# Kernel optimization log

Measured on AMD Instinct MI355X. Metric: run time of the kernel, lower is better.

## Reference

```python
import jax, jax.numpy as jnp
import numpy as np

B, NV, NE = 32, 8192, 65536
SUBSTEPS = 8
DT = 0.01
K_SPRING = 1.0e4   # spring stiffness
CG_ITERS = 20      # fixed CG iterations for the implicit solve
EPS = 1e-12


def setup_inputs() -> dict:
    key = jax.random.key(0)
    k0, k1, k2, k3, k4, k5 = jax.random.split(key, 6)
    # small actuation signals per spring (rest-length modulation)
    input_action = jax.random.normal(k0, (B, NE), dtype=jnp.float32) * 0.05
    # random spring graph with guaranteed i != j
    edge_i = jax.random.randint(k1, (NE,), 0, NV, dtype=jnp.int32)
    off = jax.random.randint(k2, (NE,), 1, NV, dtype=jnp.int32)
    edge_j = ((edge_i + off) % NV).astype(jnp.int32)
    pos0 = jax.random.normal(k3, (B, NV, 3), dtype=jnp.float32) * 0.5
    vel0 = jnp.zeros((B, NV, 3), dtype=jnp.float32)
    # rest lengths near the initial configuration so the system starts close to equilibrium
    d0 = pos0[0, edge_i] - pos0[0, edge_j]
    rest_len = jnp.linalg.norm(d0, axis=-1) + 1e-2
    mass = jax.random.uniform(k4, (NV,), dtype=jnp.float32) + 0.5
    return {"input_action": input_action, "pos0": pos0, "vel0": vel0,
            "rest_len": rest_len, "mass": mass,
            "edge_i": edge_i, "edge_j": edge_j}


def _bdot(a, b):
    # per-batch inner product, keepdims for broadcasting: [B,1,1]
    return jnp.sum(a * b, axis=(1, 2), keepdims=True)


def _spring_force(pos, rest_eff, ei, ej):
    # pos: [B,NV,3], rest_eff: [B,NE]
    d = pos[:, ei] - pos[:, ej]                       # [B,NE,3]
    l = jnp.linalg.norm(d, axis=-1, keepdims=True)    # [B,NE,1]
    dirn = d / jnp.maximum(l, 1e-6)
    fe = -K_SPRING * (l - rest_eff[..., None]) * dirn # [B,NE,3]
    f = jnp.zeros_like(pos).at[:, ei].add(fe).at[:, ej].add(-fe)
    return f


def _matvec(x, mass, ei, ej):
    # A x = M x + dt^2 * k * L x  (graph Laplacian Hessian approximation)
    d = x[:, ei] - x[:, ej]
    Lx = jnp.zeros_like(x).at[:, ei].add(d).at[:, ej].add(-d)
    return mass[None, :, None] * x + (DT * DT * K_SPRING) * Lx


def _cg_solve(b, mass, ei, ej):
    x = jnp.zeros_like(b)
    r = b
    p = r
    rs = _bdot(r, r)

    def body(carry, _):
        x, r, p, rs = carry
        Ap = _matvec(p, mass, ei, ej)
        alpha = rs / (_bdot(p, Ap) + EPS)
        x = x + alpha * p
        r = r - alpha * Ap
        rs_new = _bdot(r, r)
        p = r + (rs_new / (rs + EPS)) * p
        return (x, r, p, rs_new), None

    (x, _, _, _), _ = jax.lax.scan(body, (x, r, p, rs), None, length=CG_ITERS)
    return x


def reference(input_action, pos0, vel0, rest_len, mass, edge_i, edge_j):
    gravity = jnp.array([0.0, -9.8, 0.0], dtype=pos0.dtype)
    rest_eff = rest_len[None, :] * (1.0 + input_action)  # actuated rest lengths [B,NE]
    m3 = mass[None, :, None]

    def step(carry, _):
        pos, vel = carry
        f = _spring_force(pos, rest_eff, edge_i, edge_j) + m3 * gravity
        b = m3 * vel + DT * f                  # implicit Euler RHS
        v_new = _cg_solve(b, mass, edge_i, edge_j)
        pos_new = pos + DT * v_new
        return (pos_new, v_new), pos_new

    _, traj = jax.lax.scan(step, (pos0, vel0), None, length=SUBSTEPS)
    # traj: [SUBSTEPS, B, NV, 3] -> [B, SUBSTEPS, NV, 3]
    return jnp.transpose(traj, (1, 0, 2, 3))
```

## Files before the change

kernel.cpp:

```cpp
#include <hip/hip_runtime.h>
#include <hip/hip_cooperative_groups.h>
#include <math.h>

namespace cg = cooperative_groups;

#define NVERT 8192
#define NEDGE 65536
#define NSUB 8
#define NCG 20
#define GRID 256
#define BLOCK 1024
#define DT 0.01f
#define KS 10000.0f
#define NGRP 16
#define GSIZE 16

struct Params {
  const float* action;
  const float* pos0;
  const float* vel0;
  const float* rest_len;
  const float* mass;
  const int* edge_i;
  const int* edge_j;
  float* out;
  float4* pos;
  float4* Q0;
  float4* Q1;
  float* rest_eff;
  int* adj_off;
  int* adjE_off;
  int* row_ptr;
  int* cursor;
  double* Pd;
  double* Gd;
  unsigned* bar;
};

union U64F4 { unsigned long long u[2]; float4 f; };
union U64D  { unsigned long long u;    double d; };

__device__ __forceinline__ float4 ld_dev(const float4* p) {
  U64F4 r;
  r.u[0] = __hip_atomic_load((const unsigned long long*)p,     __ATOMIC_RELAXED, __HIP_MEMORY_SCOPE_AGENT);
  r.u[1] = __hip_atomic_load((const unsigned long long*)p + 1, __ATOMIC_RELAXED, __HIP_MEMORY_SCOPE_AGENT);
  return r.f;
}
__device__ __forceinline__ void st_dev(float4* p, float4 v) {
  U64F4 r; r.f = v;
  __hip_atomic_store((unsigned long long*)p,     r.u[0], __ATOMIC_RELAXED, __HIP_MEMORY_SCOPE_AGENT);
  __hip_atomic_store((unsigned long long*)p + 1, r.u[1], __ATOMIC_RELAXED, __HIP_MEMORY_SCOPE_AGENT);
}
__device__ __forceinline__ double lddbl_dev(const double* p) {
  U64D r;
  r.u = __hip_atomic_load((const unsigned long long*)p, __ATOMIC_RELAXED, __HIP_MEMORY_SCOPE_AGENT);
  return r.d;
}
__device__ __forceinline__ void stdbl_dev(double* p, double v) {
  U64D r; r.d = v;
  __hip_atomic_store((unsigned long long*)p, r.u, __ATOMIC_RELAXED, __HIP_MEMORY_SCOPE_AGENT);
}

__device__ __forceinline__ float4 f4(float3 a) { return make_float4(a.x, a.y, a.z, 0.f); }

__device__ __forceinline__ void fast_bar(unsigned* bar, unsigned ep) {
  __syncthreads();
  if (threadIdx.x == 0) {
    const unsigned g = blockIdx.x >> 4;
    const unsigned old = __hip_atomic_fetch_add(bar + g * 32, 1u,
                          __ATOMIC_RELAXED, __HIP_MEMORY_SCOPE_AGENT);
    if (old == GSIZE * ep - 1) {
      const unsigned old2 = __hip_atomic_fetch_add(bar + NGRP * 32, 1u,
                             __ATOMIC_RELAXED, __HIP_MEMORY_SCOPE_AGENT);
      if (old2 == NGRP * ep - 1) {
#pragma unroll
        for (int i = 0; i < NGRP; ++i)
          __hip_atomic_store(bar + (NGRP + 1 + i) * 32, ep,
                             __ATOMIC_RELAXED, __HIP_MEMORY_SCOPE_AGENT);
      }
    }
    while (__hip_atomic_load(bar + (NGRP + 1 + (blockIdx.x >> 4)) * 32,
                             __ATOMIC_RELAXED, __HIP_MEMORY_SCOPE_AGENT) < ep)
      __builtin_amdgcn_s_sleep(1);
  }
  __syncthreads();
}

__device__ __forceinline__ void fast_bar_red(unsigned* bar, unsigned ep,
                                             const double* Pd, double* Gd, int par,
                                             int* lflag) {
  __syncthreads();
  const unsigned g = blockIdx.x >> 4;
  if (threadIdx.x == 0) {
    const unsigned old = __hip_atomic_fetch_add(bar + g * 32, 1u,
                          __ATOMIC_RELAXED, __HIP_MEMORY_SCOPE_AGENT);
    *lflag = (old == GSIZE * ep - 1);
  }
  __syncthreads();
  if (*lflag) {
    if (threadIdx.x < 96) {
      const double* base = Pd + (size_t)par * 256 * 96 + (size_t)(g * GSIZE) * 96
                           + threadIdx.x;
      double s = 0.0;
#pragma unroll
      for (int j = 0; j < GSIZE; ++j) s += lddbl_dev(base + j * 96);
      stdbl_dev(&Gd[(size_t)par * NGRP * 96 + g * 96 + threadIdx.x], s);
    }
    __syncthreads();
    if (threadIdx.x == 0) {
      const unsigned old2 = __hip_atomic_fetch_add(bar + NGRP * 32, 1u,
                             __ATOMIC_RELAXED, __HIP_MEMORY_SCOPE_AGENT);
      if (old2 == NGRP * ep - 1) {
#pragma unroll
        for (int i = 0; i < NGRP; ++i)
          __hip_atomic_store(bar + (NGRP + 1 + i) * 32, ep,
                             __ATOMIC_RELAXED, __HIP_MEMORY_SCOPE_AGENT);
      }
    }
  }
  if (threadIdx.x == 0) {
    while (__hip_atomic_load(bar + (NGRP + 1 + g) * 32,
                             __ATOMIC_RELAXED, __HIP_MEMORY_SCOPE_AGENT) < ep)
      __builtin_amdgcn_s_sleep(1);
  }
  __syncthreads();
}

__device__ __forceinline__ void publish_store(double* Pd, int par, double d0, double d1,
                                              double d2, double* lds) {
  d0 += __shfl_down(d0, 32);
  d1 += __shfl_down(d1, 32);
  d2 += __shfl_down(d2, 32);
  const int lane = threadIdx.x & 63, w = threadIdx.x >> 6;
  if (lane < 32) {
    lds[w * 96 + lane] = d0;
    lds[w * 96 + 32 + lane] = d1;
    lds[w * 96 + 64 + lane] = d2;
  }
  __syncthreads();
  if (threadIdx.x < 96) {
    double s = 0.0;
#pragma unroll
    for (int ww = 0; ww < BLOCK / 64; ++ww) s += lds[ww * 96 + threadIdx.x];
    stdbl_dev(&Pd[(size_t)par * 256 * 96 + (size_t)blockIdx.x * 96 + threadIdx.x], s);
  }
}

__device__ __forceinline__ void reduce_small(const double* Gd, int par,
                                             double* lds_part, double* lds_acc) {
  const int tid = threadIdx.x;
  if (tid < NGRP * 96)
    lds_part[tid] = lddbl_dev(Gd + (size_t)par * NGRP * 96 + tid);
  __syncthreads();
  if (tid < 96) {
    double s = 0.0;
#pragma unroll
    for (int g = 0; g < NGRP; ++g) s += lds_part[g * 96 + tid];
    lds_acc[tid] = s;
  }
  __syncthreads();
}

__global__ void __launch_bounds__(BLOCK) mass_spring_kernel(Params P) {
  cg::grid_group grid = cg::this_grid();
  __shared__ double lds_red[(BLOCK / 64) * 96];
  __shared__ double lds_part[NGRP * 96];
  __shared__ double lds_acc[96];
  __shared__ int lds_scan[BLOCK];
  __shared__ int lds_flag;

  const int tid = threadIdx.x;
  const int gtid = blockIdx.x * BLOCK + tid;
  const int b = tid & 31;
  const int v = gtid >> 5;
  const int vb = v * 32 + b;
  const int b16 = b * 16, b4 = b * 4;
  unsigned ep = 0;

  for (int i = gtid; i < NEDGE * 32; i += GRID * BLOCK) {
    const int e = i >> 5, bb = i & 31;
    P.rest_eff[e * 32 + bb] = P.rest_len[e] * (1.0f + P.action[bb * NEDGE + e]);
  }
  float3 pv, vv;
  pv.x = P.pos0[(b * NVERT + v) * 3 + 0];
  pv.y = P.pos0[(b * NVERT + v) * 3 + 1];
  pv.z = P.pos0[(b * NVERT + v) * 3 + 2];
  vv.x = P.vel0[(b * NVERT + v) * 3 + 0];
  vv.y = P.vel0[(b * NVERT + v) * 3 + 1];
  vv.z = P.vel0[(b * NVERT + v) * 3 + 2];
  st_dev(&P.pos[vb], f4(pv));
  if (gtid < NVERT) P.cursor[gtid] = 0;
  if (gtid < (2 * NGRP + 1) * 32) P.bar[gtid] = 0u;
  grid.sync();

  if (gtid < NEDGE) {
    atomicAdd(&P.cursor[P.edge_i[gtid]], 1);
    atomicAdd(&P.cursor[P.edge_j[gtid]], 1);
  }
  grid.sync();

  if (blockIdx.x == 0) {
    const int base = tid * (NVERT / BLOCK);
    int loc[NVERT / BLOCK];
    int sum = 0;
#pragma unroll
    for (int i = 0; i < NVERT / BLOCK; ++i) { loc[i] = P.cursor[base + i]; sum += loc[i]; }
    lds_scan[tid] = sum;
    __syncthreads();
    for (int off = 1; off < BLOCK; off <<= 1) {
      int t = 0;
      if (tid >= off) t = lds_scan[tid - off];
      __syncthreads();
      if (tid >= off) lds_scan[tid] += t;
      __syncthreads();
    }
    int run = lds_scan[tid] - sum;
#pragma unroll
    for (int i = 0; i < NVERT / BLOCK; ++i) {
      P.row_ptr[base + i] = run;
      P.cursor[base + i] = run;
      run += loc[i];
    }
    if (tid == BLOCK - 1) P.row_ptr[NVERT] = run;
  }
  grid.sync();

  if (gtid < NEDGE) {
    const int ei = P.edge_i[gtid], ej = P.edge_j[gtid];
    const int ai = atomicAdd(&P.cursor[ei], 1);
    P.adj_off[ai] = ej * 512; P.adjE_off[ai] = gtid * 128;
    const int aj = atomicAdd(&P.cursor[ej], 1);
    P.adj_off[aj] = ei * 512; P.adjE_off[aj] = gtid * 128;
  }
  grid.sync();

  const float m_v = P.mass[v];
  const int rbeg = P.row_ptr[v], rend = P.row_ptr[v + 1];
  const float degf = (float)(rend - rbeg);

  float4* qRd = P.Q0;
  float4* qWr = P.Q1;
  int pub = 0;

  for (int s = 0; s < NSUB; ++s) {
    float fx = 0.f, fy = 0.f, fz = 0.f;
    for (int a = rbeg; a < rend; ++a) {
      const int off = P.adj_off[a];
      const float4 pu = ld_dev((const float4*)((const char*)P.pos + off + b16));
      const float re = *(const float*)((const char*)P.rest_eff + P.adjE_off[a] + b4);
      const float dx = pv.x - pu.x, dy = pv.y - pu.y, dz = pv.z - pu.z;
      const float l = sqrtf(dx * dx + dy * dy + dz * dz);
      const float coef = -KS * (l - re) / fmaxf(l, 1e-6f);
      fx += coef * dx; fy += coef * dy; fz += coef * dz;
    }
    float3 rv;
    rv.x = m_v * vv.x + DT * fx;
    rv.y = m_v * vv.y + DT * (fy - 9.8f * m_v);
    rv.z = m_v * vv.z + DT * fz;
    st_dev(&qRd[vb], f4(rv));
    float3 xacc = make_float3(0.f, 0.f, 0.f);
    float3 pc = rv;
    float3 ap;
    float3 Sr, Sp;
    fast_bar(P.bar, ++ep);

    for (int k = 0; k < NCG; ++k) {
      if (k == 0) {
        float sx = 0.f, sy = 0.f, sz = 0.f;
#pragma unroll 4
        for (int a = rbeg; a < rend; ++a) {
          const float4 qu = ld_dev((const float4*)((const char*)qRd + P.adj_off[a] + b16));
          sx += qu.x; sy += qu.y; sz += qu.z;
        }
        Sr = make_float3(sx, sy, sz);
        Sp = Sr;
        ap.x = (m_v + degf) * pc.x - Sp.x;
        ap.y = (m_v + degf) * pc.y - Sp.y;
        ap.z = (m_v + degf) * pc.z - Sp.z;
      } else {
        float sx = 0.f, sy = 0.f, sz = 0.f;
#pragma unroll 4
        for (int a = rbeg; a < rend; ++a) {
          const float4 qu = ld_dev((const float4*)((const char*)qRd + P.adj_off[a] + b16));
          sx += qu.x; sy += qu.y; sz += qu.z;
        }
        reduce_small(P.Gd, (pub + 1) & 1, lds_part, lds_acc);
        const double rsx = lds_acc[b];
        const double pq  = lds_acc[32 + b];
        const double qq  = lds_acc[64 + b];
        const float alpha = (float)(rsx / (pq + 1e-12));
        const double rs_rec = (double)alpha * (double)alpha * qq - rsx;
        const float beta = (float)(rs_rec / (rsx + 1e-12));
        xacc.x += alpha * pc.x; xacc.y += alpha * pc.y; xacc.z += alpha * pc.z;
        rv.x -= alpha * ap.x; rv.y -= alpha * ap.y; rv.z -= alpha * ap.z;
        Sr.x -= alpha * sx; Sr.y -= alpha * sy; Sr.z -= alpha * sz;
        pc.x = rv.x + beta * pc.x; pc.y = rv.y + beta * pc.y; pc.z = rv.z + beta * pc.z;
        Sp.x = Sr.x + beta * Sp.x; Sp.y = Sr.y + beta * Sp.y; Sp.z = Sr.z + beta * Sp.z;
        ap.x = (m_v + degf) * pc.x - Sp.x;
        ap.y = (m_v + degf) * pc.y - Sp.y;
        ap.z = (m_v + degf) * pc.z - Sp.z;
      }
      st_dev(&qWr[vb], f4(ap));
      publish_store(P.Pd, pub & 1,
                    (double)(rv.x * rv.x) + (double)(rv.y * rv.y) + (double)(rv.z * rv.z),
                    (double)(pc.x * ap.x) + (double)(pc.y * ap.y) + (double)(pc.z * ap.z),
                    (double)(ap.x * ap.x) + (double)(ap.y * ap.y) + (double)(ap.z * ap.z),
                    lds_red);
      fast_bar_red(P.bar, ++ep, P.Pd, P.Gd, pub & 1, &lds_flag);
      ++pub;
      float4* t = qRd; qRd = qWr; qWr = t;
    }

    {
      reduce_small(P.Gd, (pub + 1) & 1, lds_part, lds_acc);
      const double rsx = lds_acc[b];
      const double pq  = lds_acc[32 + b];
      const float alpha = (float)(rsx / (pq + 1e-12));
      xacc.x += alpha * pc.x; xacc.y += alpha * pc.y; xacc.z += alpha * pc.z;
      vv = xacc;
      pv.x += DT * vv.x; pv.y += DT * vv.y; pv.z += DT * vv.z;
      st_dev(&P.pos[vb], f4(pv));
      float* o = P.out + ((size_t)(b * NSUB + s) * NVERT + (size_t)v) * 3;
      o[0] = pv.x; o[1] = pv.y; o[2] = pv.z;
      fast_bar(P.bar, ++ep);
    }
  }
}

extern "C" void kernel_launch(void* const* d_in, const int* in_sizes, int n_in,
                              void* d_out, int out_size, void* d_ws, size_t ws_size,
                              hipStream_t stream) {
  Params P;
  P.action = (const float*)d_in[0];
  P.pos0 = (const float*)d_in[1];
  P.vel0 = (const float*)d_in[2];
  P.rest_len = (const float*)d_in[3];
  P.mass = (const float*)d_in[4];
  P.edge_i = (const int*)d_in[5];
  P.edge_j = (const int*)d_in[6];
  P.out = (float*)d_out;

  char* w = (char*)d_ws;
  auto alloc = [&](size_t bytes) {
    char* p = w;
    w += (bytes + 255) & ~(size_t)255;
    return p;
  };
  const size_t vec_bytes = (size_t)NVERT * 32 * sizeof(float4);
  P.pos = (float4*)alloc(vec_bytes);
  P.Q0  = (float4*)alloc(vec_bytes);
  P.Q1  = (float4*)alloc(vec_bytes);
  P.rest_eff = (float*)alloc((size_t)NEDGE * 32 * sizeof(float));
  P.adj_off  = (int*)alloc((size_t)2 * NEDGE * sizeof(int));
  P.adjE_off = (int*)alloc((size_t)2 * NEDGE * sizeof(int));
  P.row_ptr  = (int*)alloc((size_t)(NVERT + 1) * sizeof(int));
  P.cursor   = (int*)alloc((size_t)NVERT * sizeof(int));
  P.Pd       = (double*)alloc((size_t)2 * 256 * 96 * sizeof(double));
  P.Gd       = (double*)alloc((size_t)2 * NGRP * 96 * sizeof(double));
  P.bar      = (unsigned*)alloc((size_t)(2 * NGRP + 1) * 32 * sizeof(unsigned));

  void* args[] = { &P };
  hipLaunchCooperativeKernel(reinterpret_cast<void*>(mass_spring_kernel),
                             dim3(GRID), dim3(BLOCK), args, 0, stream);
}
```

Baseline: 2.405 ms.

## Split padded float4 vertex buffers into XY float2 and Z float arrays

Vertex position and CG search-direction buffers move from padded float4 to separate float2 (xy) and float (z) arrays. Each gather then reads 12 bytes instead of 16 and issues two atomic loads rather than two 64-bit halves of a float4. The Gd partial-sum loads for the CG reduction are now issued before the neighbour gather loop, so their latency overlaps it, and a few gather loops get unroll hints. In exchange there are more separate memory streams per gather and more pointer bookkeeping.

```diff
diff --git a/kernel.cpp b/kernel.cpp
--- a/kernel.cpp
+++ b/kernel.cpp
@@ -24,9 +24,10 @@
   const int* edge_i;
   const int* edge_j;
   float* out;
-  float4* pos;
-  float4* Q0;
-  float4* Q1;
+  float2* posXY;
+  float*  posZ;
+  float2 *QXY0, *QXY1;
+  float  *QZ0,  *QZ1;
   float* rest_eff;
   int* adj_off;
   int* adjE_off;
@@ -37,19 +38,27 @@
   unsigned* bar;
 };
 
-union U64F4 { unsigned long long u[2]; float4 f; };
-union U64D  { unsigned long long u;    double d; };
-
-__device__ __forceinline__ float4 ld_dev(const float4* p) {
-  U64F4 r;
-  r.u[0] = __hip_atomic_load((const unsigned long long*)p,     __ATOMIC_RELAXED, __HIP_MEMORY_SCOPE_AGENT);
-  r.u[1] = __hip_atomic_load((const unsigned long long*)p + 1, __ATOMIC_RELAXED, __HIP_MEMORY_SCOPE_AGENT);
+union U64F2 { unsigned long long u; float2 f; };
+union U32F  { unsigned u; float f; };
+union U64D  { unsigned long long u; double d; };
+
+__device__ __forceinline__ float2 ld2_dev(const float2* p) {
+  U64F2 r;
+  r.u = __hip_atomic_load((const unsigned long long*)p, __ATOMIC_RELAXED, __HIP_MEMORY_SCOPE_AGENT);
   return r.f;
 }
-__device__ __forceinline__ void st_dev(float4* p, float4 v) {
-  U64F4 r; r.f = v;
-  __hip_atomic_store((unsigned long long*)p,     r.u[0], __ATOMIC_RELAXED, __HIP_MEMORY_SCOPE_AGENT);
-  __hip_atomic_store((unsigned long long*)p + 1, r.u[1], __ATOMIC_RELAXED, __HIP_MEMORY_SCOPE_AGENT);
+__device__ __forceinline__ void st2_dev(float2* p, float2 v) {
+  U64F2 r; r.f = v;
+  __hip_atomic_store((unsigned long long*)p, r.u, __ATOMIC_RELAXED, __HIP_MEMORY_SCOPE_AGENT);
+}
+__device__ __forceinline__ float ldf_dev(const float* p) {
+  U32F r;
+  r.u = __hip_atomic_load((const unsigned*)p, __ATOMIC_RELAXED, __HIP_MEMORY_SCOPE_AGENT);
+  return r.f;
+}
+__device__ __forceinline__ void stf_dev(float* p, float v) {
+  U32F r; r.f = v;
+  __hip_atomic_store((unsigned*)p, r.u, __ATOMIC_RELAXED, __HIP_MEMORY_SCOPE_AGENT);
 }
 __device__ __forceinline__ double lddbl_dev(const double* p) {
   U64D r;
@@ -60,8 +69,6 @@
   U64D r; r.d = v;
   __hip_atomic_store((unsigned long long*)p, r.u, __ATOMIC_RELAXED, __HIP_MEMORY_SCOPE_AGENT);
 }
-
-__device__ __forceinline__ float4 f4(float3 a) { return make_float4(a.x, a.y, a.z, 0.f); }
 
 __device__ __forceinline__ void fast_bar(unsigned* bar, unsigned ep) {
   __syncthreads();
@@ -79,7 +86,7 @@
                              __ATOMIC_RELAXED, __HIP_MEMORY_SCOPE_AGENT);
       }
     }
-    while (__hip_atomic_load(bar + (NGRP + 1 + (blockIdx.x >> 4)) * 32,
+    while (__hip_atomic_load(bar + (NGRP + 1 + g) * 32,
                              __ATOMIC_RELAXED, __HIP_MEMORY_SCOPE_AGENT) < ep)
       __builtin_amdgcn_s_sleep(1);
   }
@@ -149,8 +156,10 @@
 __device__ __forceinline__ void reduce_small(const double* Gd, int par,
                                              double* lds_part, double* lds_acc) {
   const int tid = threadIdx.x;
-  if (tid < NGRP * 96)
-    lds_part[tid] = lddbl_dev(Gd + (size_t)par * NGRP * 96 + tid);
+  const double* base = Gd + (size_t)par * NGRP * 96;
+  lds_part[tid] = lddbl_dev(base + tid);
+  if (tid < NGRP * 96 - BLOCK)
+    lds_part[BLOCK + tid] = lddbl_dev(base + BLOCK + tid);
   __syncthreads();
   if (tid < 96) {
     double s = 0.0;
@@ -174,7 +183,7 @@
   const int b = tid & 31;
   const int v = gtid >> 5;
   const int vb = v * 32 + b;
-  const int b16 = b * 16, b4 = b * 4;
+  const int b8 = b * 8, b4 = b * 4;
   unsigned ep = 0;
 
   for (int i = gtid; i < NEDGE * 32; i += GRID * BLOCK) {
@@ -188,7 +197,8 @@
   vv.x = P.vel0[(b * NVERT + v) * 3 + 0];
   vv.y = P.vel0[(b * NVERT + v) * 3 + 1];
   vv.z = P.vel0[(b * NVERT + v) * 3 + 2];
-  st_dev(&P.pos[vb], f4(pv));
+  st2_dev(&P.posXY[vb], make_float2(pv.x, pv.y));
+  stf_dev(&P.posZ[vb], pv.z);
   if (gtid < NVERT) P.cursor[gtid] = 0;
   if (gtid < (2 * NGRP + 1) * 32) P.bar[gtid] = 0u;
   grid.sync();
@@ -228,9 +238,9 @@
   if (gtid < NEDGE) {
     const int ei = P.edge_i[gtid], ej = P.edge_j[gtid];
     const int ai = atomicAdd(&P.cursor[ei], 1);
-    P.adj_off[ai] = ej * 512; P.adjE_off[ai] = gtid * 128;
+    P.adj_off[ai] = ej * 256; P.adjE_off[ai] = gtid * 128;
     const int aj = atomicAdd(&P.cursor[ej], 1);
-    P.adj_off[aj] = ei * 512; P.adjE_off[aj] = gtid * 128;
+    P.adj_off[aj] = ei * 256; P.adjE_off[aj] = gtid * 128;
   }
   grid.sync();
 
@@ -238,17 +248,19 @@
   const int rbeg = P.row_ptr[v], rend = P.row_ptr[v + 1];
   const float degf = (float)(rend - rbeg);
 
-  float4* qRd = P.Q0;
-  float4* qWr = P.Q1;
+  float2* qXYrd = P.QXY0; float2* qXYwr = P.QXY1;
+  float*  qZrd  = P.QZ0;  float*  qZwr  = P.QZ1;
   int pub = 0;
 
   for (int s = 0; s < NSUB; ++s) {
     float fx = 0.f, fy = 0.f, fz = 0.f;
+#pragma unroll 4
     for (int a = rbeg; a < rend; ++a) {
       const int off = P.adj_off[a];
-      const float4 pu = ld_dev((const float4*)((const char*)P.pos + off + b16));
+      const float2 pxy = ld2_dev((const float2*)((const char*)P.posXY + off + b8));
+      const float  puz = ldf_dev((const float*)((const char*)P.posZ + (off >> 1) + b4));
       const float re = *(const float*)((const char*)P.rest_eff + P.adjE_off[a] + b4);
-      const float dx = pv.x - pu.x, dy = pv.y - pu.y, dz = pv.z - pu.z;
+      const float dx = pv.x - pxy.x, dy = pv.y - pxy.y, dz = pv.z - puz;
       const float l = sqrtf(dx * dx + dy * dy + dz * dz);
       const float coef = -KS * (l - re) / fmaxf(l, 1e-6f);
       fx += coef * dx; fy += coef * dy; fz += coef * dz;
@@ -257,7 +269,8 @@
     rv.x = m_v * vv.x + DT * fx;
     rv.y = m_v * vv.y + DT * (fy - 9.8f * m_v);
     rv.z = m_v * vv.z + DT * fz;
-    st_dev(&qRd[vb], f4(rv));
+    st2_dev(&qXYrd[vb], make_float2(rv.x, rv.y));
+    stf_dev(&qZrd[vb], rv.z);
     float3 xacc = make_float3(0.f, 0.f, 0.f);
     float3 pc = rv;
     float3 ap;
@@ -269,8 +282,10 @@
         float sx = 0.f, sy = 0.f, sz = 0.f;
 #pragma unroll 4
         for (int a = rbeg; a < rend; ++a) {
-          const float4 qu = ld_dev((const float4*)((const char*)qRd + P.adj_off[a] + b16));
-          sx += qu.x; sy += qu.y; sz += qu.z;
+          const int off = P.adj_off[a];
+          const float2 qxy = ld2_dev((const float2*)((const char*)qXYrd + off + b8));
+          const float  qz  = ldf_dev((const float*)((const char*)qZrd + (off >> 1) + b4));
+          sx += qxy.x; sy += qxy.y; sz += qz;
         }
         Sr = make_float3(sx, sy, sz);
         Sp = Sr;
@@ -278,13 +293,28 @@
         ap.y = (m_v + degf) * pc.y - Sp.y;
         ap.z = (m_v + degf) * pc.z - Sp.z;
       } else {
+        const double* gbase = P.Gd + (size_t)((pub + 1) & 1) * NGRP * 96;
+        const double gval0 = lddbl_dev(gbase + tid);
+        double gval1 = 0.0;
+        if (tid < NGRP * 96 - BLOCK) gval1 = lddbl_dev(gbase + BLOCK + tid);
         float sx = 0.f, sy = 0.f, sz = 0.f;
 #pragma unroll 4
         for (int a = rbeg; a < rend; ++a) {
-          const float4 qu = ld_dev((const float4*)((const char*)qRd + P.adj_off[a] + b16));
-          sx += qu.x; sy += qu.y; sz += qu.z;
+          const int off = P.adj_off[a];
+          const float2 qxy = ld2_dev((const float2*)((const char*)qXYrd + off + b8));
+          const float  qz  = ldf_dev((const float*)((const char*)qZrd + (off >> 1) + b4));
+          sx += qxy.x; sy += qxy.y; sz += qz;
         }
-        reduce_small(P.Gd, (pub + 1) & 1, lds_part, lds_acc);
+        lds_part[tid] = gval0;
+        if (tid < NGRP * 96 - BLOCK) lds_part[BLOCK + tid] = gval1;
+        __syncthreads();
+        if (tid < 96) {
+          double s = 0.0;
+#pragma unroll
+          for (int g = 0; g < NGRP; ++g) s += lds_part[g * 96 + tid];
+          lds_acc[tid] = s;
+        }
+        __syncthreads();
         const double rsx = lds_acc[b];
         const double pq  = lds_acc[32 + b];
         const double qq  = lds_acc[64 + b];
@@ -300,7 +330,8 @@
         ap.y = (m_v + degf) * pc.y - Sp.y;
         ap.z = (m_v + degf) * pc.z - Sp.z;
       }
-      st_dev(&qWr[vb], f4(ap));
+      st2_dev(&qXYwr[vb], make_float2(ap.x, ap.y));
+      stf_dev(&qZwr[vb], ap.z);
       publish_store(P.Pd, pub & 1,
                     (double)(rv.x * rv.x) + (double)(rv.y * rv.y) + (double)(rv.z * rv.z),
                     (double)(pc.x * ap.x) + (double)(pc.y * ap.y) + (double)(pc.z * ap.z),
@@ -308,7 +339,8 @@
                     lds_red);
       fast_bar_red(P.bar, ++ep, P.Pd, P.Gd, pub & 1, &lds_flag);
       ++pub;
-      float4* t = qRd; qRd = qWr; qWr = t;
+      float2* t2 = qXYrd; qXYrd = qXYwr; qXYwr = t2;
+      float*  t1 = qZrd;  qZrd  = qZwr;  qZwr  = t1;
     }
 
     {
@@ -319,7 +351,8 @@
       xacc.x += alpha * pc.x; xacc.y += alpha * pc.y; xacc.z += alpha * pc.z;
       vv = xacc;
       pv.x += DT * vv.x; pv.y += DT * vv.y; pv.z += DT * vv.z;
-      st_dev(&P.pos[vb], f4(pv));
+      st2_dev(&P.posXY[vb], make_float2(pv.x, pv.y));
+      stf_dev(&P.posZ[vb], pv.z);
       float* o = P.out + ((size_t)(b * NSUB + s) * NVERT + (size_t)v) * 3;
       o[0] = pv.x; o[1] = pv.y; o[2] = pv.z;
       fast_bar(P.bar, ++ep);
@@ -346,10 +379,14 @@
     w += (bytes + 255) & ~(size_t)255;
     return p;
   };
-  const size_t vec_bytes = (size_t)NVERT * 32 * sizeof(float4);
-  P.pos = (float4*)alloc(vec_bytes);
-  P.Q0  = (float4*)alloc(vec_bytes);
-  P.Q1  = (float4*)alloc(vec_bytes);
+  const size_t xy_bytes = (size_t)NVERT * 32 * sizeof(float2);
+  const size_t z_bytes  = (size_t)NVERT * 32 * sizeof(float);
+  P.posXY = (float2*)alloc(xy_bytes);
+  P.posZ  = (float*)alloc(z_bytes);
+  P.QXY0  = (float2*)alloc(xy_bytes);
+  P.QXY1  = (float2*)alloc(xy_bytes);
+  P.QZ0   = (float*)alloc(z_bytes);
+  P.QZ1   = (float*)alloc(z_bytes);
   P.rest_eff = (float*)alloc((size_t)NEDGE * 32 * sizeof(float));
   P.adj_off  = (int*)alloc((size_t)2 * NEDGE * sizeof(int));
   P.adjE_off = (int*)alloc((size_t)2 * NEDGE * sizeof(int));
```

Measured after the change: 2.099 ms (median of 2 runs). 12.7% less time.
